# Performance work log

Hardware: AMD Instinct MI355X
Metric: run time of the kernel (lower is better)

Reference implementation:

```python
import jax, jax.numpy as jnp
from jax import lax
import numpy as np

B, T, I, H, O = 128, 256, 256, 1024, 128


def _rnn_layer(x, W_ih, W_hh, b_ih, b_hh):
    # x: [B, T, D_in] -> hidden states [B, T, H]
    # precompute input projection for all timesteps (batched GEMM)
    xW = jnp.einsum('btd,hd->bth', x, W_ih) + b_ih + b_hh  # [B, T, H]

    def step(h, xw_t):
        h = jnp.tanh(xw_t + h @ W_hh.T)  # [B, H]
        return h, h

    h0 = jnp.zeros((x.shape[0], W_hh.shape[0]), x.dtype)
    _, hs = lax.scan(step, h0, jnp.swapaxes(xW, 0, 1))  # hs: [T, B, H]
    return jnp.swapaxes(hs, 0, 1)  # [B, T, H]


def setup_inputs() -> dict:
    key = jax.random.key(0)
    ks = jax.random.split(key, 11)
    s_ih0 = 1.0 / np.sqrt(H)
    inp = {
        'X': jax.random.normal(ks[0], (B, T, I), jnp.float32),
        'W_ih0': jax.random.uniform(ks[1], (H, I), jnp.float32, -s_ih0, s_ih0),
        'W_hh0': jax.random.uniform(ks[2], (H, H), jnp.float32, -s_ih0, s_ih0),
        'b_ih0': jax.random.uniform(ks[3], (H,), jnp.float32, -s_ih0, s_ih0),
        'b_hh0': jax.random.uniform(ks[4], (H,), jnp.float32, -s_ih0, s_ih0),
        'W_ih1': jax.random.uniform(ks[5], (H, H), jnp.float32, -s_ih0, s_ih0),
        'W_hh1': jax.random.uniform(ks[6], (H, H), jnp.float32, -s_ih0, s_ih0),
        'b_ih1': jax.random.uniform(ks[7], (H,), jnp.float32, -s_ih0, s_ih0),
        'b_hh1': jax.random.uniform(ks[8], (H,), jnp.float32, -s_ih0, s_ih0),
        'W_fc': jax.random.uniform(ks[9], (O, H), jnp.float32, -s_ih0, s_ih0),
        'b_fc': jax.random.uniform(ks[10], (O,), jnp.float32, -s_ih0, s_ih0),
    }
    return inp


def reference(X, W_ih0, W_hh0, b_ih0, b_hh0, W_ih1, W_hh1, b_ih1, b_hh1, W_fc, b_fc):
    h1 = _rnn_layer(X, W_ih0, W_hh0, b_ih0, b_hh0)   # layer 0: [B, T, H]
    h2 = _rnn_layer(h1, W_ih1, W_hh1, b_ih1, b_hh1)  # layer 1: [B, T, H]
    last = h2[:, -1, :]                               # [B, H]
    return last @ W_fc.T + b_fc                       # [B, O]
```

## Files before the change

### kernel.cpp

```cpp
#include <hip/hip_runtime.h>
#include <stdint.h>
#include <stddef.h>

#define B_ 128
#define T_ 256
#define I_ 256
#define H_ 1024
#define O_ 128

typedef __attribute__((ext_vector_type(8))) __bf16 bf16x8;
typedef __attribute__((ext_vector_type(4))) float f32x4;
typedef unsigned long long u64;



__global__ void split_kernel(const float* __restrict__ src, __bf16* __restrict__ hi,
                             __bf16* __restrict__ lo, int n) {
    int i = blockIdx.x * blockDim.x + threadIdx.x;
    int stride = gridDim.x * blockDim.x;
    for (; i < n; i += stride) {
        float v = src[i];
        __bf16 h = (__bf16)v;
        hi[i] = h;
        lo[i] = (__bf16)(v - (float)h);
    }
}

__global__ void pack_x(const float* __restrict__ X, u64* __restrict__ xp) {
    int i = blockIdx.x * 256 + threadIdx.x;
    int ln = i & 15;
    int k2 = (i >> 4) & 127;
    int bt16 = (i >> 11) & 7;
    int t = i >> 14;
    int b = bt16 * 16 + ln;
    long xo = (long)b * T_ * I_ + (long)t * I_ + k2 * 2;
    float v0 = X[xo], v1 = X[xo + 1];
    union { __bf16 b; unsigned short u; } h0, l0, h1, l1;
    h0.b = (__bf16)v0; l0.b = (__bf16)(v0 - (float)h0.b);
    h1.b = (__bf16)v1; l1.b = (__bf16)(v1 - (float)h1.b);
    u64 pk = (u64)((unsigned)h0.u | ((unsigned)l0.u << 16))
           | ((u64)((unsigned)h1.u | ((unsigned)l1.u << 16)) << 32);
    xp[(long)t * 16384 + bt16 * 2048 + k2 * 16 + ln] = pk;
}

__global__ void bias_sum_kernel(const float* __restrict__ a, const float* __restrict__ b,
                                float* __restrict__ o, int n) {
    int i = blockIdx.x * blockDim.x + threadIdx.x;
    if (i < n) o[i] = a[i] + b[i];
}

__global__ void transpose_fc(const float* __restrict__ w, float* __restrict__ wt) {
    int i = blockIdx.x * blockDim.x + threadIdx.x;
    if (i < O_ * H_) {
        int o = i / H_, k = i - o * H_;
        wt[k * O_ + o] = w[i];
    }
}


__device__ __forceinline__ void unpack4(const u64* d, bf16x8* hi, bf16x8* lo) {
    union { unsigned u[4]; bf16x8 v; } Hh, Ll;
    #pragma unroll
    for (int i = 0; i < 4; ++i) {
        unsigned lo32 = (unsigned)d[i], hi32 = (unsigned)(d[i] >> 32);
        Hh.u[i] = (lo32 & 0xFFFFu) | (hi32 << 16);
        Ll.u[i] = (lo32 >> 16) | (hi32 & 0xFFFF0000u);
    }
    *hi = Hh.v; *lo = Ll.v;
}

__device__ __forceinline__ void load_swz(const u64* p, bf16x8* hi, bf16x8* lo) {
    u64 d[4];
    #pragma unroll
    for (int i = 0; i < 4; ++i)
        d[i] = __hip_atomic_load((u64*)p + i * 16, __ATOMIC_RELAXED,
                                 __HIP_MEMORY_SCOPE_AGENT);
    unpack4(d, hi, lo);
}

__device__ __forceinline__ void load_swz_cached(const u64* p, bf16x8* hi, bf16x8* lo) {
    u64 d[4];
    #pragma unroll
    for (int i = 0; i < 4; ++i)
        d[i] = p[i * 16];
    unpack4(d, hi, lo);
}

template <int CPW, int SEG0CH, bool CACHED0>
__device__ __forceinline__ void step_full(
    const u64* __restrict__ A0,
    const u64* __restrict__ Sp,
    const bf16x8 (&wh)[CPW][2], const bf16x8 (&wl)[CPW][2],
    const float* __restrict__ bs,
    u64* __restrict__ So, u64* __restrict__ Qo,
    int bt, int jt, int w, float* red)
{
    const int lane = threadIdx.x & 63;
    const int ln = lane & 15;
    const int q  = lane >> 4;

    f32x4 acc[2][2][3];
    #pragma unroll
    for (int s = 0; s < 2; ++s)
        #pragma unroll
        for (int n = 0; n < 2; ++n)
            #pragma unroll
            for (int r = 0; r < 3; ++r)
                acc[s][n][r] = (f32x4){0.f, 0.f, 0.f, 0.f};

    #pragma unroll
    for (int c = 0; c < CPW; ++c) {
        int gC = w * CPW + c;
        bf16x8 ah[2], al[2];
        if (gC < SEG0CH) {
            const u64* base = A0 + (long)(gC * 16 + q * 4) * 16 + ln;
            #pragma unroll
            for (int s = 0; s < 2; ++s) {
                const u64* p = base + (long)(bt * 2 + s) * (SEG0CH * 256);
                if (CACHED0) load_swz_cached(p, &ah[s], &al[s]);
                else         load_swz(p, &ah[s], &al[s]);
            }
        } else {
            const u64* base = Sp + (long)((gC - SEG0CH) * 16 + q * 4) * 16 + ln;
            #pragma unroll
            for (int s = 0; s < 2; ++s)
                load_swz(base + (long)(bt * 2 + s) * 8192, &ah[s], &al[s]);
        }
        #pragma unroll
        for (int s = 0; s < 2; ++s)
            #pragma unroll
            for (int n = 0; n < 2; ++n) {
                acc[s][n][0] = __builtin_amdgcn_mfma_f32_16x16x32_bf16(ah[s], wh[c][n], acc[s][n][0], 0, 0, 0);
                acc[s][n][1] = __builtin_amdgcn_mfma_f32_16x16x32_bf16(al[s], wh[c][n], acc[s][n][1], 0, 0, 0);
                acc[s][n][2] = __builtin_amdgcn_mfma_f32_16x16x32_bf16(ah[s], wl[c][n], acc[s][n][2], 0, 0, 0);
            }
    }

    {
        float* my = red + w * 1056;
        #pragma unroll
        for (int s = 0; s < 2; ++s)
            #pragma unroll
            for (int n = 0; n < 2; ++n) {
                f32x4 sum = acc[s][n][0] + acc[s][n][1] + acc[s][n][2];
                #pragma unroll
                for (int r = 0; r < 4; ++r)
                    my[(s * 16 + q * 4 + r) * 33 + n * 16 + ln] = sum[r];
            }
    }
    __syncthreads();

    {
        int tid = threadIdx.x;
        int row = tid & 31;
        int jp  = tid >> 5;
        int c0 = jp * 2;
        float v0 = 0.f, v1 = 0.f;
        #pragma unroll
        for (int w8 = 0; w8 < 8; ++w8) {
            v0 += red[w8 * 1056 + row * 33 + c0];
            v1 += red[w8 * 1056 + row * 33 + c0 + 1];
        }
        int j0 = jt * 32 + c0;
        float h0 = tanhf(v0 + bs[j0]);
        float h1v = tanhf(v1 + bs[j0 + 1]);
        union { __bf16 b; unsigned short u; } x0h, x0l, x1h, x1l;
        x0h.b = (__bf16)h0;  x0l.b = (__bf16)(h0 - (float)x0h.b);
        x1h.b = (__bf16)h1v; x1l.b = (__bf16)(h1v - (float)x1h.b);
        u64 pk = (u64)((unsigned)x0h.u | ((unsigned)x0l.u << 16))
               | ((u64)((unsigned)x1h.u | ((unsigned)x1l.u << 16)) << 32);
        long idx = (long)(bt * 2 + (row >> 4)) * 8192 + (long)(jt * 16 + jp) * 16 + (row & 15);
        __hip_atomic_store(&So[idx], pk, __ATOMIC_RELAXED, __HIP_MEMORY_SCOPE_AGENT);
        if (Qo)
            __hip_atomic_store(&Qo[idx], pk, __ATOMIC_RELAXED, __HIP_MEMORY_SCOPE_AGENT);
    }
}

__device__ __forceinline__ void grid_barrier(unsigned* bar, int grp, unsigned step) {
    asm volatile("s_waitcnt vmcnt(0)" ::: "memory");
    __syncthreads();
    if (threadIdx.x == 0) {
        unsigned tgt = step + 1u;
        unsigned old = __hip_atomic_fetch_add(&bar[grp * 32], 1u, __ATOMIC_RELAXED,
                                              __HIP_MEMORY_SCOPE_AGENT);
        if ((old & 31u) == 31u) {
            unsigned so = __hip_atomic_fetch_add(&bar[256], 1u, __ATOMIC_RELAXED,
                                                 __HIP_MEMORY_SCOPE_AGENT);
            if ((so & 7u) == 7u) {
                #pragma unroll
                for (int i = 0; i < 8; ++i)
                    __hip_atomic_store(&bar[512 + i * 32], tgt, __ATOMIC_RELAXED,
                                       __HIP_MEMORY_SCOPE_AGENT);
            }
        }
        while (__hip_atomic_load(&bar[512 + grp * 32], __ATOMIC_RELAXED,
                                 __HIP_MEMORY_SCOPE_AGENT) < tgt)
            __builtin_amdgcn_s_sleep(2);
    }
    __syncthreads();
    asm volatile("" ::: "memory");
}

struct PArgs {
    const u64* xp;
    const __bf16 *Wi0h, *Wi0l, *Wr0h, *Wr0l;
    const __bf16 *Wi1h, *Wi1l, *Wr1h, *Wr1l;
    const float *bs0, *bs1;
    u64 *h1;
    u64 *s0a, *s0b, *s1a, *s1b;
    unsigned* bar;
};

__global__ __launch_bounds__(512, 2) void persistent_rnn(PArgs a) {
    __shared__ float red[8 * 1056];
    const int w = threadIdx.x >> 6;
    const int lane = threadIdx.x & 63;
    const int ln = lane & 15;
    const int q  = lane >> 4;
    const int grp = blockIdx.x & 7;
    const int layer = blockIdx.x >> 7;
    const int r7 = blockIdx.x & 127;
    const int jt = r7 & 31;
    const int bt = r7 >> 5;

    if (layer == 0) {
        bf16x8 wh[5][2], wl[5][2];
        #pragma unroll
        for (int c = 0; c < 5; ++c) {
            int gC = w * 5 + c;
            #pragma unroll
            for (int n = 0; n < 2; ++n) {
                int jr = jt * 32 + n * 16 + ln;
                if (gC < 8) {
                    wh[c][n] = *(const bf16x8*)(a.Wi0h + (long)jr * 256 + gC * 32 + q * 8);
                    wl[c][n] = *(const bf16x8*)(a.Wi0l + (long)jr * 256 + gC * 32 + q * 8);
                } else {
                    wh[c][n] = *(const bf16x8*)(a.Wr0h + (long)jr * 1024 + (gC - 8) * 32 + q * 8);
                    wl[c][n] = *(const bf16x8*)(a.Wr0l + (long)jr * 1024 + (gC - 8) * 32 + q * 8);
                }
            }
        }
        for (int t = 0; t <= T_; ++t) {
            if (t < T_) {
                const u64* sin = (t & 1) ? a.s0b : a.s0a;
                u64* sout      = (t & 1) ? a.s0a : a.s0b;
                step_full<5, 8, true>(a.xp + (long)t * 16384, sin, wh, wl, a.bs0,
                                      sout, a.h1 + (long)t * 65536, bt, jt, w, red);
            }
            grid_barrier(a.bar, grp, (unsigned)t);
        }
    } else {
        bf16x8 wh[8][2], wl[8][2];
        #pragma unroll
        for (int c = 0; c < 8; ++c) {
            int gC = w * 8 + c;
            #pragma unroll
            for (int n = 0; n < 2; ++n) {
                int jr = jt * 32 + n * 16 + ln;
                if (gC < 32) {
                    wh[c][n] = *(const bf16x8*)(a.Wi1h + (long)jr * 1024 + gC * 32 + q * 8);
                    wl[c][n] = *(const bf16x8*)(a.Wi1l + (long)jr * 1024 + gC * 32 + q * 8);
                } else {
                    wh[c][n] = *(const bf16x8*)(a.Wr1h + (long)jr * 1024 + (gC - 32) * 32 + q * 8);
                    wl[c][n] = *(const bf16x8*)(a.Wr1l + (long)jr * 1024 + (gC - 32) * 32 + q * 8);
                }
            }
        }
        for (int t = 0; t <= T_; ++t) {
            if (t >= 1) {
                int t1 = t - 1;
                const u64* sin = (t1 & 1) ? a.s1b : a.s1a;
                u64* sout      = (t1 & 1) ? a.s1a : a.s1b;
                step_full<8, 32, false>(a.h1 + (long)t1 * 65536, sin, wh, wl, a.bs1,
                                        sout, (u64*)nullptr, bt, jt, w, red);
            }
            grid_barrier(a.bar, grp, (unsigned)t);
        }
    }
}

__global__ __launch_bounds__(128) void fc_kernel(const u64* __restrict__ sp,
                                                 const float* __restrict__ wt,
                                                 const float* __restrict__ bfc,
                                                 float* __restrict__ out) {
    int b = blockIdx.x;
    int o = threadIdx.x;
    int bt = b >> 4, r = b & 15;
    float acc = 0.f;
    #pragma unroll 4
    for (int k2 = 0; k2 < H_ / 2; ++k2) {
        u64 pk = __hip_atomic_load((u64*)sp + (long)bt * 8192 + (long)k2 * 16 + r,
                                   __ATOMIC_RELAXED, __HIP_MEMORY_SCOPE_AGENT);
        union { unsigned short u; __bf16 bf; } hh, hl;
        unsigned lo32 = (unsigned)pk, hi32 = (unsigned)(pk >> 32);
        hh.u = (unsigned short)(lo32 & 0xFFFF); hl.u = (unsigned short)(lo32 >> 16);
        float x0 = (float)hh.bf + (float)hl.bf;
        hh.u = (unsigned short)(hi32 & 0xFFFF); hl.u = (unsigned short)(hi32 >> 16);
        float x1 = (float)hh.bf + (float)hl.bf;
        acc += x0 * wt[(2 * k2) * O_ + o] + x1 * wt[(2 * k2 + 1) * O_ + o];
    }
    out[b * O_ + o] = acc + bfc[o];
}


extern "C" void kernel_launch(void* const* d_in, const int* in_sizes, int n_in,
                              void* d_out, int out_size, void* d_ws, size_t ws_size,
                              hipStream_t stream) {
    const float* X     = (const float*)d_in[0];
    const float* Wih0  = (const float*)d_in[1];
    const float* Whh0  = (const float*)d_in[2];
    const float* bih0  = (const float*)d_in[3];
    const float* bhh0  = (const float*)d_in[4];
    const float* Wih1  = (const float*)d_in[5];
    const float* Whh1  = (const float*)d_in[6];
    const float* bih1  = (const float*)d_in[7];
    const float* bhh1  = (const float*)d_in[8];
    const float* Wfc   = (const float*)d_in[9];
    const float* bfc   = (const float*)d_in[10];
    float* out = (float*)d_out;

    char* p = (char*)d_ws;
    auto alloc = [&](size_t bytes) -> void* {
        void* r = (void*)p;
        p += (bytes + 255) & ~(size_t)255;
        return r;
    };
    const size_t nW0 = (size_t)H_ * I_;
    const size_t nW  = (size_t)H_ * H_;
    u64* xp      = (u64*)alloc((size_t)T_ * 16384 * 8);
    __bf16* W0h  = (__bf16*)alloc(nW0 * 2);
    __bf16* W0l  = (__bf16*)alloc(nW0 * 2);
    __bf16* Wh0h = (__bf16*)alloc(nW * 2);
    __bf16* Wh0l = (__bf16*)alloc(nW * 2);
    __bf16* Wi1h = (__bf16*)alloc(nW * 2);
    __bf16* Wi1l = (__bf16*)alloc(nW * 2);
    __bf16* Wh1h = (__bf16*)alloc(nW * 2);
    __bf16* Wh1l = (__bf16*)alloc(nW * 2);
    u64* h1   = (u64*)alloc((size_t)T_ * 65536 * 8);
    u64* s0a  = (u64*)alloc(65536 * 8);
    u64* s0b  = (u64*)alloc(65536 * 8);
    u64* s1a  = (u64*)alloc(65536 * 8);
    u64* s1b  = (u64*)alloc(65536 * 8);
    float* wfct = (float*)alloc((size_t)H_ * O_ * 4);
    float* bs0  = (float*)alloc((size_t)H_ * 4);
    float* bs1  = (float*)alloc((size_t)H_ * 4);
    unsigned* bar = (unsigned*)alloc(4096);
    (void)ws_size; (void)n_in; (void)in_sizes; (void)out_size;

    pack_x<<<16384, 256, 0, stream>>>(X, xp);
    split_kernel<<<512, 256, 0, stream>>>(Wih0, W0h, W0l, (int)nW0);
    split_kernel<<<1024, 256, 0, stream>>>(Whh0, Wh0h, Wh0l, (int)nW);
    split_kernel<<<1024, 256, 0, stream>>>(Wih1, Wi1h, Wi1l, (int)nW);
    split_kernel<<<1024, 256, 0, stream>>>(Whh1, Wh1h, Wh1l, (int)nW);
    bias_sum_kernel<<<4, 256, 0, stream>>>(bih0, bhh0, bs0, H_);
    bias_sum_kernel<<<4, 256, 0, stream>>>(bih1, bhh1, bs1, H_);
    transpose_fc<<<(O_ * H_ + 255) / 256, 256, 0, stream>>>(Wfc, wfct);

    hipMemsetAsync(s0a, 0, 65536 * 8, stream);
    hipMemsetAsync(s1a, 0, 65536 * 8, stream);
    hipMemsetAsync(bar, 0, 4096, stream);

    PArgs args;
    args.xp = xp;
    args.Wi0h = W0h; args.Wi0l = W0l; args.Wr0h = Wh0h; args.Wr0l = Wh0l;
    args.Wi1h = Wi1h; args.Wi1l = Wi1l; args.Wr1h = Wh1h; args.Wr1l = Wh1l;
    args.bs0 = bs0; args.bs1 = bs1;
    args.h1 = h1;
    args.s0a = s0a; args.s0b = s0b; args.s1a = s1a; args.s1b = s1b;
    args.bar = bar;
    void* kp[] = { &args };
    hipLaunchCooperativeKernel((void*)persistent_rnn, dim3(256), dim3(512), kp, 0, stream);

    fc_kernel<<<B_, O_, 0, stream>>>(s1a, wfct, bfc, out);
}
```

Measured before the change: 2.161 ms.

## Split grid barrier into per-batch-tile domains, drop h1 history buffer, prefetch loads

```diff
diff --git a/kernel.cpp b/kernel.cpp
--- a/kernel.cpp
+++ b/kernel.cpp
@@ -69,30 +69,13 @@
     *hi = Hh.v; *lo = Ll.v;
 }
 
-__device__ __forceinline__ void load_swz(const u64* p, bf16x8* hi, bf16x8* lo) {
-    u64 d[4];
-    #pragma unroll
-    for (int i = 0; i < 4; ++i)
-        d[i] = __hip_atomic_load((u64*)p + i * 16, __ATOMIC_RELAXED,
-                                 __HIP_MEMORY_SCOPE_AGENT);
-    unpack4(d, hi, lo);
-}
-
-__device__ __forceinline__ void load_swz_cached(const u64* p, bf16x8* hi, bf16x8* lo) {
-    u64 d[4];
-    #pragma unroll
-    for (int i = 0; i < 4; ++i)
-        d[i] = p[i * 16];
-    unpack4(d, hi, lo);
-}
-
 template <int CPW, int SEG0CH, bool CACHED0>
 __device__ __forceinline__ void step_full(
     const u64* __restrict__ A0,
     const u64* __restrict__ Sp,
     const bf16x8 (&wh)[CPW][2], const bf16x8 (&wl)[CPW][2],
     const float* __restrict__ bs,
-    u64* __restrict__ So, u64* __restrict__ Qo,
+    u64* __restrict__ So,
     int bt, int jt, int w, float* red)
 {
     const int lane = threadIdx.x & 63;
@@ -108,24 +91,46 @@
             for (int r = 0; r < 3; ++r)
                 acc[s][n][r] = (f32x4){0.f, 0.f, 0.f, 0.f};
 
+    constexpr int PF = 2;
+    u64 d[PF][2][4];
+
+    auto issue = [&](int c, u64 (&dst)[2][4]) {
+        const int gC = w * CPW + c;
+        if (gC < SEG0CH) {
+            const u64* base = A0 + (long)(gC * 16 + q * 4) * 16 + ln;
+            #pragma unroll
+            for (int s = 0; s < 2; ++s) {
+                const u64* p = base + (long)(bt * 2 + s) * (SEG0CH * 256);
+                #pragma unroll
+                for (int i = 0; i < 4; ++i) {
+                    if (CACHED0) dst[s][i] = p[i * 16];
+                    else dst[s][i] = __hip_atomic_load((u64*)p + i * 16,
+                                         __ATOMIC_RELAXED, __HIP_MEMORY_SCOPE_AGENT);
+                }
+            }
+        } else {
+            const u64* base = Sp + (long)((gC - SEG0CH) * 16 + q * 4) * 16 + ln;
+            #pragma unroll
+            for (int s = 0; s < 2; ++s) {
+                const u64* p = base + (long)(bt * 2 + s) * 8192;
+                #pragma unroll
+                for (int i = 0; i < 4; ++i)
+                    dst[s][i] = __hip_atomic_load((u64*)p + i * 16,
+                                    __ATOMIC_RELAXED, __HIP_MEMORY_SCOPE_AGENT);
+            }
+        }
+    };
+
+    issue(0, d[0]);
+    issue(1, d[1]);
+
     #pragma unroll
     for (int c = 0; c < CPW; ++c) {
-        int gC = w * CPW + c;
         bf16x8 ah[2], al[2];
-        if (gC < SEG0CH) {
-            const u64* base = A0 + (long)(gC * 16 + q * 4) * 16 + ln;
-            #pragma unroll
-            for (int s = 0; s < 2; ++s) {
-                const u64* p = base + (long)(bt * 2 + s) * (SEG0CH * 256);
-                if (CACHED0) load_swz_cached(p, &ah[s], &al[s]);
-                else         load_swz(p, &ah[s], &al[s]);
-            }
-        } else {
-            const u64* base = Sp + (long)((gC - SEG0CH) * 16 + q * 4) * 16 + ln;
-            #pragma unroll
-            for (int s = 0; s < 2; ++s)
-                load_swz(base + (long)(bt * 2 + s) * 8192, &ah[s], &al[s]);
-        }
+        #pragma unroll
+        for (int s = 0; s < 2; ++s)
+            unpack4(d[c & 1][s], &ah[s], &al[s]);
+        if (c + PF < CPW) issue(c + PF, d[c & 1]);
         #pragma unroll
         for (int s = 0; s < 2; ++s)
             #pragma unroll
@@ -171,30 +176,22 @@
                | ((u64)((unsigned)x1h.u | ((unsigned)x1l.u << 16)) << 32);
         long idx = (long)(bt * 2 + (row >> 4)) * 8192 + (long)(jt * 16 + jp) * 16 + (row & 15);
         __hip_atomic_store(&So[idx], pk, __ATOMIC_RELAXED, __HIP_MEMORY_SCOPE_AGENT);
-        if (Qo)
-            __hip_atomic_store(&Qo[idx], pk, __ATOMIC_RELAXED, __HIP_MEMORY_SCOPE_AGENT);
-    }
-}
-
-__device__ __forceinline__ void grid_barrier(unsigned* bar, int grp, unsigned step) {
+    }
+}
+
+__device__ __forceinline__ void domain_barrier(unsigned* bar, int dom, unsigned step) {
     asm volatile("s_waitcnt vmcnt(0)" ::: "memory");
     __syncthreads();
     if (threadIdx.x == 0) {
-        unsigned tgt = step + 1u;
-        unsigned old = __hip_atomic_fetch_add(&bar[grp * 32], 1u, __ATOMIC_RELAXED,
+        unsigned* cnt = &bar[dom * 64];
+        unsigned* rel = &bar[dom * 64 + 32];
+        unsigned old = __hip_atomic_fetch_add(cnt, 1u, __ATOMIC_RELAXED,
                                               __HIP_MEMORY_SCOPE_AGENT);
-        if ((old & 31u) == 31u) {
-            unsigned so = __hip_atomic_fetch_add(&bar[256], 1u, __ATOMIC_RELAXED,
-                                                 __HIP_MEMORY_SCOPE_AGENT);
-            if ((so & 7u) == 7u) {
-                #pragma unroll
-                for (int i = 0; i < 8; ++i)
-                    __hip_atomic_store(&bar[512 + i * 32], tgt, __ATOMIC_RELAXED,
-                                       __HIP_MEMORY_SCOPE_AGENT);
-            }
-        }
-        while (__hip_atomic_load(&bar[512 + grp * 32], __ATOMIC_RELAXED,
-                                 __HIP_MEMORY_SCOPE_AGENT) < tgt)
+        if (old == step * 64u + 63u)
+            __hip_atomic_store(rel, step + 1u, __ATOMIC_RELAXED,
+                               __HIP_MEMORY_SCOPE_AGENT);
+        while (__hip_atomic_load(rel, __ATOMIC_RELAXED,
+                                 __HIP_MEMORY_SCOPE_AGENT) <= step)
             __builtin_amdgcn_s_sleep(2);
     }
     __syncthreads();
@@ -206,7 +203,6 @@
     const __bf16 *Wi0h, *Wi0l, *Wr0h, *Wr0l;
     const __bf16 *Wi1h, *Wi1l, *Wr1h, *Wr1l;
     const float *bs0, *bs1;
-    u64 *h1;
     u64 *s0a, *s0b, *s1a, *s1b;
     unsigned* bar;
 };
@@ -217,7 +213,6 @@
     const int lane = threadIdx.x & 63;
     const int ln = lane & 15;
     const int q  = lane >> 4;
-    const int grp = blockIdx.x & 7;
     const int layer = blockIdx.x >> 7;
     const int r7 = blockIdx.x & 127;
     const int jt = r7 & 31;
@@ -245,9 +240,9 @@
                 const u64* sin = (t & 1) ? a.s0b : a.s0a;
                 u64* sout      = (t & 1) ? a.s0a : a.s0b;
                 step_full<5, 8, true>(a.xp + (long)t * 16384, sin, wh, wl, a.bs0,
-                                      sout, a.h1 + (long)t * 65536, bt, jt, w, red);
-            }
-            grid_barrier(a.bar, grp, (unsigned)t);
+                                      sout, bt, jt, w, red);
+            }
+            domain_barrier(a.bar, bt, (unsigned)t);
         }
     } else {
         bf16x8 wh[8][2], wl[8][2];
@@ -269,12 +264,13 @@
         for (int t = 0; t <= T_; ++t) {
             if (t >= 1) {
                 int t1 = t - 1;
-                const u64* sin = (t1 & 1) ? a.s1b : a.s1a;
-                u64* sout      = (t1 & 1) ? a.s1a : a.s1b;
-                step_full<8, 32, false>(a.h1 + (long)t1 * 65536, sin, wh, wl, a.bs1,
-                                        sout, (u64*)nullptr, bt, jt, w, red);
-            }
-            grid_barrier(a.bar, grp, (unsigned)t);
+                const u64* h1in = (t1 & 1) ? a.s0a : a.s0b;
+                const u64* sin  = (t1 & 1) ? a.s1b : a.s1a;
+                u64* sout       = (t1 & 1) ? a.s1a : a.s1b;
+                step_full<8, 32, false>(h1in, sin, wh, wl, a.bs1,
+                                        sout, bt, jt, w, red);
+            }
+            domain_barrier(a.bar, bt, (unsigned)t);
         }
     }
 }
@@ -336,7 +332,6 @@
     __bf16* Wi1l = (__bf16*)alloc(nW * 2);
     __bf16* Wh1h = (__bf16*)alloc(nW * 2);
     __bf16* Wh1l = (__bf16*)alloc(nW * 2);
-    u64* h1   = (u64*)alloc((size_t)T_ * 65536 * 8);
     u64* s0a  = (u64*)alloc(65536 * 8);
     u64* s0b  = (u64*)alloc(65536 * 8);
     u64* s1a  = (u64*)alloc(65536 * 8);
@@ -365,7 +360,6 @@
     args.Wi0h = W0h; args.Wi0l = W0l; args.Wr0h = Wh0h; args.Wr0l = Wh0l;
     args.Wi1h = Wi1h; args.Wi1l = Wi1l; args.Wr1h = Wh1h; args.Wr1l = Wh1l;
     args.bs0 = bs0; args.bs1 = bs1;
-    args.h1 = h1;
     args.s0a = s0a; args.s0b = s0b; args.s1a = s1a; args.s1b = s1b;
     args.bar = bar;
     void* kp[] = { &args };
```

Result: faster. 1.971 ms (-8.8%).
